# Kernel optimization log

Measured on AMD Instinct MI355X. Metric: run time of the kernel, lower is better.

Reference implementation:

```python
import jax, jax.numpy as jnp
import numpy as np

NUM_ENT_CLASS = 150
NORMED_REL_VEC_DIST = False


def box_cxcywh_to_xyxy(b):
    cx, cy, w, h = b[..., 0], b[..., 1], b[..., 2], b[..., 3]
    return jnp.stack([cx - 0.5 * w, cy - 0.5 * h, cx + 0.5 * w, cy + 0.5 * h], axis=-1)


def box_xyxy_to_cxcywh(b):
    x0, y0, x1, y1 = b[..., 0], b[..., 1], b[..., 2], b[..., 3]
    return jnp.stack([(x0 + x1) * 0.5, (y0 + y1) * 0.5, x1 - x0, y1 - y0], axis=-1)


def generalized_box_iou(a, b):
    # a: [N,4], b: [M,4], xyxy -> [N,M]
    area_a = (a[:, 2] - a[:, 0]) * (a[:, 3] - a[:, 1])
    area_b = (b[:, 2] - b[:, 0]) * (b[:, 3] - b[:, 1])
    lt = jnp.maximum(a[:, None, :2], b[None, :, :2])
    rb = jnp.minimum(a[:, None, 2:], b[None, :, 2:])
    wh = jnp.clip(rb - lt, 0.0)
    inter = wh[..., 0] * wh[..., 1]
    union = area_a[:, None] + area_b[None, :] - inter
    iou = inter / union
    lt_c = jnp.minimum(a[:, None, :2], b[None, :, :2])
    rb_c = jnp.maximum(a[:, None, 2:], b[None, :, 2:])
    wh_c = jnp.clip(rb_c - lt_c, 0.0)
    area_c = wh_c[..., 0] * wh_c[..., 1]
    return iou - (area_c - union) / area_c


def cdist_l2(a, b):
    # a: [N,C], b: [M,C] -> [N,M] euclidean distance (gram-matrix form)
    d2 = (jnp.sum(a * a, -1)[:, None] + jnp.sum(b * b, -1)[None, :]
          - 2.0 * (a @ b.T))
    return jnp.sqrt(jnp.maximum(d2, 1e-12))


def _per_image(ent_box_n, ent_logits, ro_logits, rs_logits, ro_box_n, rs_box_n,
               rel_vec_n, scale):
    # scale: [4] = [w, h, w, h]
    ent_box = box_cxcywh_to_xyxy(ent_box_n) * scale[None, :]           # [Ne,4] pixels
    ent_cnter = box_xyxy_to_cxcywh(ent_box)[..., :2]                    # [Ne,2]
    ent_cnter_normed = ent_box_n[..., :2]

    # num_ent_class (150) != logits dim (151) -> softmax, drop background
    ro_dist = jax.nn.softmax(ro_logits, axis=-1)[..., :-1]              # [Nr,150]
    rs_dist = jax.nn.softmax(rs_logits, axis=-1)[..., :-1]
    ent_prob = jax.nn.softmax(ent_logits, axis=-1)[..., :-1]            # [Ne,150]
    ent_score = jnp.max(ent_prob, axis=-1)                              # [Ne]

    ro_box = box_cxcywh_to_xyxy(ro_box_n) * scale[None, :]              # [Nr,4]
    rs_box = box_cxcywh_to_xyxy(rs_box_n) * scale[None, :]
    rel_vec = rel_vec_n * scale[None, :]                                # [Nr,4]

    if NORMED_REL_VEC_DIST:
        vec, sc, oc = rel_vec_n, ent_cnter_normed, ent_cnter_normed
    else:
        vec, sc, oc = rel_vec, ent_cnter, ent_cnter

    # L1 distance of rel-vector endpoints to entity centers -> [Nr,Ne]
    dist_s = (jnp.abs(vec[:, None, 0] - sc[None, :, 0])
              + jnp.abs(vec[:, None, 1] - sc[None, :, 1]))
    dist_o = (jnp.abs(vec[:, None, 2] - oc[None, :, 0])
              + jnp.abs(vec[:, None, 3] - oc[None, :, 1]))
    match_vec_sub = 1.0 / (dist_s + 1.0)
    match_vec_obj = 1.0 / (dist_o + 1.0)

    m_s = ent_score[None, :] * match_vec_sub                            # conf-weighted
    m_o = ent_score[None, :] * match_vec_obj

    sub_giou = jnp.clip(generalized_box_iou(ent_box, rs_box), 0.0)      # [Ne,Nr]
    obj_giou = jnp.clip(generalized_box_iou(ent_box, ro_box), 0.0)

    sub_cls = 1.0 / (cdist_l2(rs_dist, ent_prob) + 1.0)                 # [Nr,Ne]
    obj_cls = 1.0 / (cdist_l2(ro_dist, ent_prob) + 1.0)

    dist_s_final = m_s * sub_cls * sub_giou.T                           # [Nr,Ne]
    dist_o_final = m_o * obj_cls * obj_giou.T
    return dist_s_final, dist_o_final


def setup_inputs() -> dict:
    key = jax.random.key(0)
    ks = jax.random.split(key, 8)
    B, Ne, Nr, C1 = 64, 500, 500, NUM_ENT_CLASS + 1
    inp = {
        "pred_boxes": jax.random.uniform(ks[0], (B, Ne, 4), jnp.float32),
        "pred_logits": jax.random.normal(ks[1], (B, Ne, C1), jnp.float32),
        "pred_rel_obj_logits": jax.random.normal(ks[2], (B, Nr, C1), jnp.float32),
        "pred_rel_sub_logits": jax.random.normal(ks[3], (B, Nr, C1), jnp.float32),
        "pred_rel_obj_box": jax.random.uniform(ks[4], (B, Nr, 4), jnp.float32),
        "pred_rel_sub_box": jax.random.uniform(ks[5], (B, Nr, 4), jnp.float32),
        "pred_rel_vec": jax.random.uniform(ks[6], (B, Nr, 4), jnp.float32),
        "target_sizes": 600.0 + 600.0 * jax.random.uniform(ks[7], (B, 2), jnp.float32),
    }
    return inp


def reference(pred_boxes, pred_logits, pred_rel_obj_logits, pred_rel_sub_logits,
              pred_rel_obj_box, pred_rel_sub_box, pred_rel_vec, target_sizes):
    img_h, img_w = target_sizes[:, 0], target_sizes[:, 1]
    scale_fct = jnp.stack([img_w, img_h, img_w, img_h], axis=1)  # [B,4]
    sub_dist, obj_dist = jax.vmap(_per_image)(
        pred_boxes, pred_logits, pred_rel_obj_logits, pred_rel_sub_logits,
        pred_rel_obj_box, pred_rel_sub_box, pred_rel_vec, scale_fct)
    return sub_dist, obj_dist
```

## Files before the change

kernel.cpp:

```cpp
#include <hip/hip_runtime.h>
#include <math.h>

#define NB   64
#define NPT  500
#define C1   151
#define CM1  150
#define EAF  12
#define RAF  20

#define GRP_ELEMS  2560
#define IMG_ELEMS  (32 * GRP_ELEMS)
#define PROB_ELEMS ((size_t)NB * IMG_ELEMS)

typedef __bf16 bf16x8 __attribute__((ext_vector_type(8)));
typedef float  f32x4  __attribute__((ext_vector_type(4)));

__device__ __forceinline__ float rcpf(float x) { return __builtin_amdgcn_rcpf(x); }
__device__ __forceinline__ float rsqf(float x) { return __builtin_amdgcn_rsqf(x); }

extern "C" __global__ void __launch_bounds__(256)
k_pre(const float* __restrict__ boxes, const float* __restrict__ ent_logits,
      const float* __restrict__ ro_logits, const float* __restrict__ rs_logits,
      const float* __restrict__ ro_box, const float* __restrict__ rs_box,
      const float* __restrict__ rel_vec, const float* __restrict__ tsz,
      __bf16* __restrict__ entP, __bf16* __restrict__ rsP, __bf16* __restrict__ roP,
      float* __restrict__ entAux, float* __restrict__ relAux)
{
    const int tid = threadIdx.x;
    const int q   = tid & 15;
    const int rl  = tid >> 4;
    const int bx  = blockIdx.x;
    const int set = bx / 2000;
    const int rowIdx = (bx - set * 2000) * 16 + rl;
    const int b = rowIdx / 500;
    const int i = rowIdx - b * 500;

    const float* src = (set == 0 ? ent_logits : (set == 1 ? rs_logits : ro_logits))
                       + (size_t)rowIdx * C1;

    float x[10];
    #pragma unroll
    for (int t = 0; t < 9; ++t) x[t] = src[q + 16 * t];
    x[9] = (q <= 6) ? src[q + 144] : -INFINITY;

    float mAll = x[0];
    #pragma unroll
    for (int t = 1; t < 10; ++t) mAll = fmaxf(mAll, x[t]);
    float mKept = x[0];
    #pragma unroll
    for (int t = 1; t < 9; ++t) mKept = fmaxf(mKept, x[t]);
    if (q <= 5) mKept = fmaxf(mKept, x[9]);

    #pragma unroll
    for (int off = 1; off < 16; off <<= 1) {
        mAll  = fmaxf(mAll,  __shfl_xor(mAll,  off, 16));
        mKept = fmaxf(mKept, __shfl_xor(mKept, off, 16));
    }

    float e[10], s = 0.f, s2 = 0.f;
    #pragma unroll
    for (int t = 0; t < 9; ++t) {
        e[t] = __expf(x[t] - mAll);
        s  += e[t];
        s2 += e[t] * e[t];
    }
    e[9] = (q <= 6) ? __expf(x[9] - mAll) : 0.f;
    s += e[9];
    if (q <= 5) s2 += e[9] * e[9];

    #pragma unroll
    for (int off = 1; off < 16; off <<= 1) {
        s  += __shfl_xor(s,  off, 16);
        s2 += __shfl_xor(s2, off, 16);
    }

    const float inv = rcpf(s);
    const float pm  = __expf(mKept - mAll) * inv;
    const float nn  = s2 * inv * inv;

    __bf16* dstT = (set == 0 ? entP : (set == 1 ? rsP : roP));
    const int g  = i >> 4, ir = i & 15;
    __bf16* dst = dstT + ((size_t)b * 32 + g) * GRP_ELEMS + ir * 8 + (q & 7);
    const int qh = q >> 3;
    #pragma unroll
    for (int t = 0; t < 9; ++t)
        dst[(2 * t + qh) * 128] = (__bf16)(e[t] * inv);
    dst[(18 + qh) * 128] = (q <= 5) ? (__bf16)(e[9] * inv) : (__bf16)0.f;

    if (q == 0) {
        const float hh = tsz[b * 2 + 0];
        const float ww = tsz[b * 2 + 1];
        if (set == 0) {
            const float* bb = boxes + (size_t)rowIdx * 4;
            const float cx = bb[0], cy = bb[1], bw = bb[2], bh = bb[3];
            const float X0 = (cx - 0.5f * bw) * ww, Y0 = (cy - 0.5f * bh) * hh;
            const float X1 = (cx + 0.5f * bw) * ww, Y1 = (cy + 0.5f * bh) * hh;
            float* A = entAux + (size_t)rowIdx * EAF;
            A[0] = pm;
            A[1] = 0.5f * (X0 + X1);
            A[2] = 0.5f * (Y0 + Y1);
            A[3] = nn;
            A[4] = X0; A[5] = Y0; A[6] = X1; A[7] = Y1;
            A[8] = (X1 - X0) * (Y1 - Y0);
        } else if (set == 1) {
            const float* bb = rs_box  + (size_t)rowIdx * 4;
            const float* vv = rel_vec + (size_t)rowIdx * 4;
            const float cx = bb[0], cy = bb[1], bw = bb[2], bh = bb[3];
            float* A = relAux + (size_t)rowIdx * RAF;
            const float X0 = (cx - 0.5f * bw) * ww, Y0 = (cy - 0.5f * bh) * hh;
            const float X1 = (cx + 0.5f * bw) * ww, Y1 = (cy + 0.5f * bh) * hh;
            A[0] = X0; A[1] = Y0; A[2] = X1; A[3] = Y1;
            A[8]  = vv[0] * ww; A[9]  = vv[1] * hh;
            A[10] = vv[2] * ww; A[11] = vv[3] * hh;
            A[12] = nn;
            A[14] = (X1 - X0) * (Y1 - Y0);
        } else {
            const float* bb = ro_box + (size_t)rowIdx * 4;
            const float cx = bb[0], cy = bb[1], bw = bb[2], bh = bb[3];
            float* A = relAux + (size_t)rowIdx * RAF;
            const float X0 = (cx - 0.5f * bw) * ww, Y0 = (cy - 0.5f * bh) * hh;
            const float X1 = (cx + 0.5f * bw) * ww, Y1 = (cy + 0.5f * bh) * hh;
            A[4] = X0; A[5] = Y0; A[6] = X1; A[7] = Y1;
            A[13] = nn;
            A[15] = (X1 - X0) * (Y1 - Y0);
        }
    }
}

template <bool FULL>
__device__ __forceinline__ void epilogue(
    const float (*eA)[EAF], const float (*rA)[RAF],
    const f32x4* accS, const f32x4* accO,
    int lr, int kq, int wv, int b, int e0T, int r0T,
    float* __restrict__ outS, float* __restrict__ outO)
{
    f32x4 ev0[4], ev1[4];
    float eArea[4];
    #pragma unroll
    for (int et = 0; et < 4; ++et) {
        const float* ep = eA[et * 16 + lr];
        ev0[et] = *(const f32x4*)(ep);
        ev1[et] = *(const f32x4*)(ep + 4);
        eArea[et] = ep[8];
    }

    const unsigned baseR0 = ((unsigned)b * NPT + (unsigned)(r0T + wv * 16 + kq * 4)) * NPT;
    const unsigned eBase  = (unsigned)(e0T + lr);

    #pragma unroll
    for (int reg = 0; reg < 4; ++reg) {
        const int rIdx = wv * 16 + kq * 4 + reg;
        const bool rOK = FULL || (r0T + rIdx < NPT);
        const float* rp = rA[rIdx];
        const f32x4 rsB = *(const f32x4*)(rp);
        const f32x4 roB = *(const f32x4*)(rp + 4);
        const f32x4 vv  = *(const f32x4*)(rp + 8);
        const f32x4 rn  = *(const f32x4*)(rp + 12);
        const unsigned rowOff = baseR0 + (unsigned)reg * NPT;

        #pragma unroll
        for (int et = 0; et < 4; ++et) {
            const float score = ev0[et][0], ecx = ev0[et][1], ecy = ev0[et][2], en2 = ev0[et][3];
            const float ex0 = ev1[et][0], ey0 = ev1[et][1], ex1 = ev1[et][2], ey1 = ev1[et][3];
            const float aE = eArea[et];

            const float iwS = fmaxf(fminf(ex1, rsB[2]) - fmaxf(ex0, rsB[0]), 0.f);
            const float ihS = fmaxf(fminf(ey1, rsB[3]) - fmaxf(ey0, rsB[1]), 0.f);
            const float inS = iwS * ihS;
            const float unS = aE + rn[2] - inS;
            const float aCS = (fmaxf(ex1, rsB[2]) - fminf(ex0, rsB[0]))
                            * (fmaxf(ey1, rsB[3]) - fminf(ey0, rsB[1]));
            const float gS  = fmaxf(fmaf(inS, rcpf(unS), fmaf(unS, rcpf(aCS), -1.f)), 0.f);

            const float iwO = fmaxf(fminf(ex1, roB[2]) - fmaxf(ex0, roB[0]), 0.f);
            const float ihO = fmaxf(fminf(ey1, roB[3]) - fmaxf(ey0, roB[1]), 0.f);
            const float inO = iwO * ihO;
            const float unO = aE + rn[3] - inO;
            const float aCO = (fmaxf(ex1, roB[2]) - fminf(ex0, roB[0]))
                            * (fmaxf(ey1, roB[3]) - fminf(ey0, roB[1]));
            const float gO  = fmaxf(fmaf(inO, rcpf(unO), fmaf(unO, rcpf(aCO), -1.f)), 0.f);

            const float d2s = fmaxf(fmaf(-2.f, accS[et][reg], rn[0] + en2), 1e-12f);
            const float d2o = fmaxf(fmaf(-2.f, accO[et][reg], rn[1] + en2), 1e-12f);
            const float dS  = d2s * rsqf(d2s);
            const float dO  = d2o * rsqf(d2o);
            const float distS = fabsf(vv[0] - ecx) + fabsf(vv[1] - ecy);
            const float distO = fabsf(vv[2] - ecx) + fabsf(vv[3] - ecy);
            const float qS = rcpf((distS + 1.f) * (dS + 1.f));
            const float qO = rcpf((distO + 1.f) * (dO + 1.f));

            const float vS = score * qS * gS;
            const float vO = score * qO * gO;

            const unsigned o = rowOff + eBase + (unsigned)(et * 16);
            if (FULL || (rOK && (int)(eBase + et * 16) < NPT)) {
                outS[o] = vS;
                outO[o] = vO;
            }
        }
    }
}

extern "C" __global__ void __launch_bounds__(256, 4)
k_main(const __bf16* __restrict__ entP, const __bf16* __restrict__ rsP,
       const __bf16* __restrict__ roP, const float* __restrict__ eAuxG,
       const float* __restrict__ rAuxG,
       float* __restrict__ outS, float* __restrict__ outO)
{
    __shared__ __align__(16) float eA[64][EAF];
    __shared__ __align__(16) float rA[64][RAF];

    const int tid = threadIdx.x;
    const int b   = blockIdx.x;
    const int e0T = (blockIdx.y & 7) * 64;
    const int r0T = (blockIdx.y >> 3) * 64;

    {
        const float4 z = {0.f, 0.f, 0.f, 0.f};
        for (int t = tid; t < 64 * (EAF / 4); t += 256) {
            const int e = t / (EAF / 4), qq = t % (EAF / 4);
            const int ge = e0T + e;
            ((float4*)eA[e])[qq] = (ge < NPT)
                ? ((const float4*)(eAuxG + ((size_t)b * NPT + ge) * EAF))[qq] : z;
        }
        for (int t = tid; t < 64 * (RAF / 4); t += 256) {
            const int r = t / (RAF / 4), qq = t % (RAF / 4);
            const int gr = r0T + r;
            ((float4*)rA[r])[qq] = (gr < NPT)
                ? ((const float4*)(rAuxG + ((size_t)b * NPT + gr) * RAF))[qq] : z;
        }
    }
    __syncthreads();

    const int wv   = tid >> 6;
    const int lane = tid & 63;
    const int lr   = lane & 15;
    const int kq   = lane >> 4;

    const int gR = (r0T >> 4) + wv;
    const int gE = (e0T >> 4);
    const __bf16* rsBase = rsP  + ((size_t)b * 32 + gR) * GRP_ELEMS + lr * 8;
    const __bf16* roBase = roP  + ((size_t)b * 32 + gR) * GRP_ELEMS + lr * 8;
    const __bf16* enBase = entP + ((size_t)b * 32 + gE) * GRP_ELEMS + lr * 8;

    f32x4 accS[4] = {{0,0,0,0},{0,0,0,0},{0,0,0,0},{0,0,0,0}};
    f32x4 accO[4] = {{0,0,0,0},{0,0,0,0},{0,0,0,0},{0,0,0,0}};

    #pragma unroll
    for (int ks = 0; ks < 5; ++ks) {
        const int kOff = (ks * 4 + kq) * 128;
        const bf16x8 ars = *(const bf16x8*)(rsBase + kOff);
        const bf16x8 aro = *(const bf16x8*)(roBase + kOff);
        #pragma unroll
        for (int et = 0; et < 4; ++et) {
            const bf16x8 be = *(const bf16x8*)(enBase + et * GRP_ELEMS + kOff);
            accS[et] = __builtin_amdgcn_mfma_f32_16x16x32_bf16(ars, be, accS[et], 0, 0, 0);
            accO[et] = __builtin_amdgcn_mfma_f32_16x16x32_bf16(aro, be, accO[et], 0, 0, 0);
        }
    }

    if (e0T + 64 <= NPT && r0T + 64 <= NPT) {
        epilogue<true >(eA, rA, accS, accO, lr, kq, wv, b, e0T, r0T, outS, outO);
    } else {
        epilogue<false>(eA, rA, accS, accO, lr, kq, wv, b, e0T, r0T, outS, outO);
    }
}

extern "C" void kernel_launch(void* const* d_in, const int* in_sizes, int n_in,
                              void* d_out, int out_size, void* d_ws, size_t ws_size,
                              hipStream_t stream)
{
    const float* boxes      = (const float*)d_in[0];
    const float* ent_logits = (const float*)d_in[1];
    const float* ro_logits  = (const float*)d_in[2];
    const float* rs_logits  = (const float*)d_in[3];
    const float* ro_box     = (const float*)d_in[4];
    const float* rs_box     = (const float*)d_in[5];
    const float* rel_vec    = (const float*)d_in[6];
    const float* tsz        = (const float*)d_in[7];

    __bf16* entP = (__bf16*)d_ws;
    __bf16* rsP  = entP + PROB_ELEMS;
    __bf16* roP  = rsP  + PROB_ELEMS;
    float*  eAux = (float*)(roP + PROB_ELEMS);
    float*  rAux = eAux + (size_t)NB * NPT * EAF;

    float* outS = (float*)d_out;
    float* outO = outS + (size_t)NB * NPT * NPT;

    hipLaunchKernelGGL(k_pre, dim3(6000), dim3(256), 0, stream,
                       boxes, ent_logits, ro_logits, rs_logits,
                       ro_box, rs_box, rel_vec, tsz,
                       entP, rsP, roP, eAux, rAux);

    hipLaunchKernelGGL(k_main, dim3(64, 64), dim3(256), 0, stream,
                       entP, rsP, roP, eAux, rAux, outS, outO);
}
```

Measured before the change: 235.7 us.

## Transpose MFMA operands so each lane stores four contiguous outputs as float4

The entity and relation operands of the MFMA are swapped, so each lane's accumulator registers now hold four consecutive entity columns for one relation row instead of four rows. The epilogue is reorganized around this: relation aux data is loaded once per lane, entity aux is read per register, and results are written with 16-byte float4 stores instead of scalar stores. This is meant to reduce the number of store instructions and improve write coalescing on a large, output-bound result. Launch bounds also raise the occupancy hint from 4 to 6 blocks, which may force register pressure or spills. NPT=500 is a multiple of 4, so the row-offset alignment of the float4 stores looks safe.

```diff
diff --git a/kernel.cpp b/kernel.cpp
--- a/kernel.cpp
+++ b/kernel.cpp
@@ -134,35 +134,30 @@
     int lr, int kq, int wv, int b, int e0T, int r0T,
     float* __restrict__ outS, float* __restrict__ outO)
 {
-    f32x4 ev0[4], ev1[4];
-    float eArea[4];
+    const int rIdx = wv * 16 + lr;
+    const int gr   = r0T + rIdx;
+    const float* rp = rA[rIdx];
+    const f32x4 rsB = *(const f32x4*)(rp);
+    const f32x4 roB = *(const f32x4*)(rp + 4);
+    const f32x4 vv  = *(const f32x4*)(rp + 8);
+    const f32x4 rn  = *(const f32x4*)(rp + 12);
+    const bool rOK  = FULL || (gr < NPT);
+    const unsigned rowOff = ((unsigned)b * NPT + (unsigned)gr) * NPT;
+
     #pragma unroll
     for (int et = 0; et < 4; ++et) {
-        const float* ep = eA[et * 16 + lr];
-        ev0[et] = *(const f32x4*)(ep);
-        ev1[et] = *(const f32x4*)(ep + 4);
-        eArea[et] = ep[8];
-    }
-
-    const unsigned baseR0 = ((unsigned)b * NPT + (unsigned)(r0T + wv * 16 + kq * 4)) * NPT;
-    const unsigned eBase  = (unsigned)(e0T + lr);
-
-    #pragma unroll
-    for (int reg = 0; reg < 4; ++reg) {
-        const int rIdx = wv * 16 + kq * 4 + reg;
-        const bool rOK = FULL || (r0T + rIdx < NPT);
-        const float* rp = rA[rIdx];
-        const f32x4 rsB = *(const f32x4*)(rp);
-        const f32x4 roB = *(const f32x4*)(rp + 4);
-        const f32x4 vv  = *(const f32x4*)(rp + 8);
-        const f32x4 rn  = *(const f32x4*)(rp + 12);
-        const unsigned rowOff = baseR0 + (unsigned)reg * NPT;
-
+        float4 vS, vO;
+        float* pS = (float*)&vS;
+        float* pO = (float*)&vO;
         #pragma unroll
-        for (int et = 0; et < 4; ++et) {
-            const float score = ev0[et][0], ecx = ev0[et][1], ecy = ev0[et][2], en2 = ev0[et][3];
-            const float ex0 = ev1[et][0], ey0 = ev1[et][1], ex1 = ev1[et][2], ey1 = ev1[et][3];
-            const float aE = eArea[et];
+        for (int reg = 0; reg < 4; ++reg) {
+            const int eIdx = et * 16 + kq * 4 + reg;
+            const float* ep = eA[eIdx];
+            const f32x4 ev0 = *(const f32x4*)(ep);
+            const f32x4 ev1 = *(const f32x4*)(ep + 4);
+            const float aE  = ep[8];
+            const float score = ev0[0], ecx = ev0[1], ecy = ev0[2], en2 = ev0[3];
+            const float ex0 = ev1[0], ey0 = ev1[1], ex1 = ev1[2], ey1 = ev1[3];
 
             const float iwS = fmaxf(fminf(ex1, rsB[2]) - fmaxf(ex0, rsB[0]), 0.f);
             const float ihS = fmaxf(fminf(ey1, rsB[3]) - fmaxf(ey0, rsB[1]), 0.f);
@@ -189,19 +184,19 @@
             const float qS = rcpf((distS + 1.f) * (dS + 1.f));
             const float qO = rcpf((distO + 1.f) * (dO + 1.f));
 
-            const float vS = score * qS * gS;
-            const float vO = score * qO * gO;
-
-            const unsigned o = rowOff + eBase + (unsigned)(et * 16);
-            if (FULL || (rOK && (int)(eBase + et * 16) < NPT)) {
-                outS[o] = vS;
-                outO[o] = vO;
-            }
-        }
-    }
-}
-
-extern "C" __global__ void __launch_bounds__(256, 4)
+            pS[reg] = score * qS * gS;
+            pO[reg] = score * qO * gO;
+        }
+        const int eBase = e0T + et * 16 + kq * 4;
+        if (rOK && (FULL || eBase < NPT)) {
+            const unsigned o = rowOff + (unsigned)eBase;
+            *(float4*)(outS + o) = vS;
+            *(float4*)(outO + o) = vO;
+        }
+    }
+}
+
+extern "C" __global__ void __launch_bounds__(256, 6)
 k_main(const __bf16* __restrict__ entP, const __bf16* __restrict__ rsP,
        const __bf16* __restrict__ roP, const float* __restrict__ eAuxG,
        const float* __restrict__ rAuxG,
@@ -249,13 +244,13 @@
     #pragma unroll
     for (int ks = 0; ks < 5; ++ks) {
         const int kOff = (ks * 4 + kq) * 128;
-        const bf16x8 ars = *(const bf16x8*)(rsBase + kOff);
-        const bf16x8 aro = *(const bf16x8*)(roBase + kOff);
+        const bf16x8 brs = *(const bf16x8*)(rsBase + kOff);
+        const bf16x8 bro = *(const bf16x8*)(roBase + kOff);
         #pragma unroll
         for (int et = 0; et < 4; ++et) {
-            const bf16x8 be = *(const bf16x8*)(enBase + et * GRP_ELEMS + kOff);
-            accS[et] = __builtin_amdgcn_mfma_f32_16x16x32_bf16(ars, be, accS[et], 0, 0, 0);
-            accO[et] = __builtin_amdgcn_mfma_f32_16x16x32_bf16(aro, be, accO[et], 0, 0, 0);
+            const bf16x8 ae = *(const bf16x8*)(enBase + et * GRP_ELEMS + kOff);
+            accS[et] = __builtin_amdgcn_mfma_f32_16x16x32_bf16(ae, brs, accS[et], 0, 0, 0);
+            accO[et] = __builtin_amdgcn_mfma_f32_16x16x32_bf16(ae, bro, accO[et], 0, 0, 0);
         }
     }
 
```

Result: slower. 296.3 us (+25.7%).

## Stage entity tile in LDS via async global_load_lds and prefetch relation fragments

Applied to the files above, without the earlier changes.

Each block now loads its shared 64-entity bf16 tile once into LDS with direct global-to-LDS loads. Before, every wave fetched that same tile from global memory on its own. The relation A fragments are prefetched into registers before the aux-table staging and barrier, so load latency overlaps with that setup. The GIoU expression is also rewritten to use one reciprocal instead of two. The cost is 20KB more LDS per block, which may limit occupancy, and the merged reciprocal may change rounding slightly or overflow for large pixel areas.

```diff
diff --git a/kernel.cpp b/kernel.cpp
--- a/kernel.cpp
+++ b/kernel.cpp
@@ -170,7 +170,7 @@
             const float unS = aE + rn[2] - inS;
             const float aCS = (fmaxf(ex1, rsB[2]) - fminf(ex0, rsB[0]))
                             * (fmaxf(ey1, rsB[3]) - fminf(ey0, rsB[1]));
-            const float gS  = fmaxf(fmaf(inS, rcpf(unS), fmaf(unS, rcpf(aCS), -1.f)), 0.f);
+            const float gS  = fmaxf(fmaf(fmaf(inS, aCS, unS * unS), rcpf(unS * aCS), -1.f), 0.f);
 
             const float iwO = fmaxf(fminf(ex1, roB[2]) - fmaxf(ex0, roB[0]), 0.f);
             const float ihO = fmaxf(fminf(ey1, roB[3]) - fmaxf(ey0, roB[1]), 0.f);
@@ -178,7 +178,7 @@
             const float unO = aE + rn[3] - inO;
             const float aCO = (fmaxf(ex1, roB[2]) - fminf(ex0, roB[0]))
                             * (fmaxf(ey1, roB[3]) - fminf(ey0, roB[1]));
-            const float gO  = fmaxf(fmaf(inO, rcpf(unO), fmaf(unO, rcpf(aCO), -1.f)), 0.f);
+            const float gO  = fmaxf(fmaf(fmaf(inO, aCO, unO * unO), rcpf(unO * aCO), -1.f), 0.f);
 
             const float d2s = fmaxf(fmaf(-2.f, accS[et][reg], rn[0] + en2), 1e-12f);
             const float d2o = fmaxf(fmaf(-2.f, accO[et][reg], rn[1] + en2), 1e-12f);
@@ -207,6 +207,7 @@
        const float* __restrict__ rAuxG,
        float* __restrict__ outS, float* __restrict__ outO)
 {
+    __shared__ __align__(16) __bf16 sEnt[4 * GRP_ELEMS];
     __shared__ __align__(16) float eA[64][EAF];
     __shared__ __align__(16) float rA[64][RAF];
 
@@ -214,6 +215,36 @@
     const int b   = blockIdx.x;
     const int e0T = (blockIdx.y & 7) * 64;
     const int r0T = (blockIdx.y >> 3) * 64;
+
+    const int wv   = tid >> 6;
+    const int lane = tid & 63;
+    const int lr   = lane & 15;
+    const int kq   = lane >> 4;
+
+    const int gR = (r0T >> 4) + wv;
+    const int gE = (e0T >> 4);
+    const __bf16* rsBase = rsP  + ((size_t)b * 32 + gR) * GRP_ELEMS + lr * 8;
+    const __bf16* roBase = roP  + ((size_t)b * 32 + gR) * GRP_ELEMS + lr * 8;
+    const __bf16* entSrc = entP + ((size_t)b * 32 + gE) * GRP_ELEMS;
+
+    bf16x8 ars[5], aro[5];
+    #pragma unroll
+    for (int ks = 0; ks < 5; ++ks) {
+        const int kOff = (ks * 4 + kq) * 128;
+        ars[ks] = *(const bf16x8*)(rsBase + kOff);
+        aro[ks] = *(const bf16x8*)(roBase + kOff);
+    }
+
+    #pragma unroll
+    for (int it = 0; it < 5; ++it) {
+        const int off = it * 4096 + wv * 1024;
+        __builtin_amdgcn_global_load_lds(
+            (const __attribute__((address_space(1))) unsigned int*)
+                ((const char*)entSrc + off + lane * 16),
+            (__attribute__((address_space(3))) unsigned int*)
+                ((char*)sEnt + off),
+            16, 0, 0);
+    }
 
     {
         const float4 z = {0.f, 0.f, 0.f, 0.f};
@@ -232,30 +263,17 @@
     }
     __syncthreads();
 
-    const int wv   = tid >> 6;
-    const int lane = tid & 63;
-    const int lr   = lane & 15;
-    const int kq   = lane >> 4;
-
-    const int gR = (r0T >> 4) + wv;
-    const int gE = (e0T >> 4);
-    const __bf16* rsBase = rsP  + ((size_t)b * 32 + gR) * GRP_ELEMS + lr * 8;
-    const __bf16* roBase = roP  + ((size_t)b * 32 + gR) * GRP_ELEMS + lr * 8;
-    const __bf16* enBase = entP + ((size_t)b * 32 + gE) * GRP_ELEMS + lr * 8;
-
     f32x4 accS[4] = {{0,0,0,0},{0,0,0,0},{0,0,0,0},{0,0,0,0}};
     f32x4 accO[4] = {{0,0,0,0},{0,0,0,0},{0,0,0,0},{0,0,0,0}};
 
     #pragma unroll
     for (int ks = 0; ks < 5; ++ks) {
-        const int kOff = (ks * 4 + kq) * 128;
-        const bf16x8 ars = *(const bf16x8*)(rsBase + kOff);
-        const bf16x8 aro = *(const bf16x8*)(roBase + kOff);
+        const int kOff = (ks * 4 + kq) * 128 + lr * 8;
         #pragma unroll
         for (int et = 0; et < 4; ++et) {
-            const bf16x8 be = *(const bf16x8*)(enBase + et * GRP_ELEMS + kOff);
-            accS[et] = __builtin_amdgcn_mfma_f32_16x16x32_bf16(ars, be, accS[et], 0, 0, 0);
-            accO[et] = __builtin_amdgcn_mfma_f32_16x16x32_bf16(aro, be, accO[et], 0, 0, 0);
+            const bf16x8 be = *(const bf16x8*)&sEnt[et * GRP_ELEMS + kOff];
+            accS[et] = __builtin_amdgcn_mfma_f32_16x16x32_bf16(ars[ks], be, accS[et], 0, 0, 0);
+            accO[et] = __builtin_amdgcn_mfma_f32_16x16x32_bf16(aro[ks], be, accO[et], 0, 0, 0);
         }
     }
 
```

Result: no change. 235.0 us (-0.3%).
